# Performance work log

Hardware: AMD Instinct MI355X
Metric: run time of the kernel (lower is better)

## Reference

```python
import jax, jax.numpy as jnp
import numpy as np

B, N, C, H = 8, 4096, 512, 8
HD = C // H  # head_dim = 64
SCALE = HD ** -0.5


def setup_inputs() -> dict:
    key = jax.random.key(0)
    k1, k2, k3, k4 = jax.random.split(key, 4)
    x1 = jax.random.normal(k1, (B, N, C), dtype=jnp.float32)
    x2 = jax.random.normal(k2, (B, N, C), dtype=jnp.float32)
    # nn.Linear(dim, 2*dim, bias=False) weights; stored as [in, out] for x @ W
    lim = 1.0 / np.sqrt(C)
    W_kv1 = jax.random.uniform(k3, (C, 2 * C), dtype=jnp.float32, minval=-lim, maxval=lim)
    W_kv2 = jax.random.uniform(k4, (C, 2 * C), dtype=jnp.float32, minval=-lim, maxval=lim)
    return {"x1": x1, "x2": x2, "W_kv1": W_kv1, "W_kv2": W_kv2}


def _heads(t):
    # [B, N, C] -> [B, H, N, HD]
    return t.reshape(B, N, H, HD).transpose(0, 2, 1, 3)


def _kv(x, W):
    kv = (x @ W).reshape(B, N, 2, H, HD)  # [B, N, 2, H, HD]
    kv = kv.transpose(2, 0, 3, 1, 4)      # [2, B, H, N, HD]
    return kv[0], kv[1]


def _ctx(k, v):
    # K^T V: [B, H, HD, HD], scaled then softmax over axis -2 (the k-feature axis)
    ctx = jnp.einsum("bhnd,bhne->bhde", k, v) * SCALE
    return jax.nn.softmax(ctx, axis=-2)


def reference(x1, x2, W_kv1, W_kv2):
    q1 = _heads(x1)
    q2 = _heads(x2)
    k1, v1 = _kv(x1, W_kv1)
    k2, v2 = _kv(x2, W_kv2)
    ctx1 = _ctx(k1, v1)
    ctx2 = _ctx(k2, v2)
    # cross: q1 attends via ctx2, q2 via ctx1
    o1 = jnp.einsum("bhnd,bhde->bhne", q1, ctx2).transpose(0, 2, 1, 3).reshape(B, N, C)
    o2 = jnp.einsum("bhnd,bhde->bhne", q2, ctx1).transpose(0, 2, 1, 3).reshape(B, N, C)
    return o1, o2
```

## Files before the change

kernel.cpp:

```cpp
#include <hip/hip_runtime.h>
#include <stdint.h>
#include <stddef.h>

#define NB 8
#define NSEQ 4096
#define NC 512
#define NH 8
#define SWZ(c) ((((c) >> 2) ^ (c)) & 7)

typedef __attribute__((ext_vector_type(4))) float f4;
typedef __attribute__((ext_vector_type(8))) short bf8;
typedef __attribute__((ext_vector_type(4))) short bf4;
typedef __attribute__((ext_vector_type(2))) unsigned int u32x2;
typedef __attribute__((ext_vector_type(4))) unsigned int u32x4;

__device__ __forceinline__ short f2bf(float f) {
  union { float f; unsigned int u; } v; v.f = f;
  unsigned int u = v.u + 0x7FFFu + ((v.u >> 16) & 1u);
  return (short)(u >> 16);
}
__device__ __forceinline__ float bf2f(short h) {
  union { unsigned int u; float f; } v;
  v.u = ((unsigned int)(unsigned short)h) << 16;
  return v.f;
}
__device__ __forceinline__ unsigned int cvtpk(float a, float b) {
  unsigned int r;
  asm("v_cvt_pk_bf16_f32 %0, %1, %2" : "=v"(r) : "v"(a), "v"(b));
  return r;
}

__global__ __launch_bounds__(256) void k_wt(const float* __restrict__ W0,
                                            const float* __restrict__ W1,
                                            short* __restrict__ Wth,
                                            short* __restrict__ Wtl) {
  __shared__ float t[64 * 65];
  int bid = blockIdx.x;
  int ot = bid & 15;
  int ct = (bid >> 4) & 7;
  int s = bid >> 7;
  const float* W = s ? W1 : W0;
  const float* src = W + (size_t)(ct * 64) * 1024 + ot * 64;
  int tid = threadIdx.x;
  int rr = tid >> 4, c4 = (tid & 15) * 4;
#pragma unroll
  for (int p = 0; p < 4; ++p) {
    int c = p * 16 + rr;
    f4 v = *(const f4*)&src[(size_t)c * 1024 + c4];
#pragma unroll
    for (int i = 0; i < 4; ++i) t[(c4 + i) * 65 + c] = v[i];
  }
  __syncthreads();
  size_t obase = (size_t)s * 524288 + (size_t)(ot * 64) * 512 + ct * 64;
#pragma unroll
  for (int p = 0; p < 4; ++p) {
    int o = p * 16 + rr;
    bf4 vh, vl;
#pragma unroll
    for (int i = 0; i < 4; ++i) {
      float v = t[o * 65 + c4 + i];
      short h = f2bf(v);
      vh[i] = h; vl[i] = f2bf(v - bf2f(h));
    }
    *(bf4*)&Wth[obase + (size_t)o * 512 + c4] = vh;
    *(bf4*)&Wtl[obase + (size_t)o * 512 + c4] = vl;
  }
}

__global__ __launch_bounds__(256) void k_xbt(const float* __restrict__ x0,
                                             const float* __restrict__ x1,
                                             short* __restrict__ XbT) {
  __shared__ short t[64 * 64];
  int bx = blockIdx.x;
  int ct = bx & 7;
  int nt = (bx >> 3) & 63;
  int b  = (bx >> 9) & 7;
  int s  = bx >> 12;
  const float* x = s ? x1 : x0;
  const float* xb = x + ((size_t)b * NSEQ + (size_t)nt * 64) * NC + ct * 64;
  int tid = threadIdx.x;
  int c4 = (tid & 15) * 4;
  int nb = (tid >> 4) * 4;
  int g = nb >> 3;
  int nlo = nb & 7;
  f4 v[4];
#pragma unroll
  for (int i = 0; i < 4; ++i)
    v[i] = *(const f4*)&xb[(size_t)(nb + i) * NC + c4];
#pragma unroll
  for (int ci = 0; ci < 4; ++ci) {
    int c = c4 + ci;
    int soff = c * 64 + ((g ^ SWZ(c)) << 3) + nlo;
    u32x2 wa;
    wa[0] = cvtpk(v[0][ci], v[1][ci]);
    wa[1] = cvtpk(v[2][ci], v[3][ci]);
    *(u32x2*)&t[soff] = wa;
  }
  __syncthreads();
  int gg = tid & 7;
  int cr = tid >> 3;
  short* Xp = XbT + ((size_t)(s * 8 + b) * NC + (size_t)ct * 64) * NSEQ + (size_t)nt * 64;
#pragma unroll
  for (int p = 0; p < 2; ++p) {
    int c = cr + p * 32;
    bf8 vv = *(const bf8*)&t[c * 64 + ((gg ^ SWZ(c)) << 3)];
    *(bf8*)&Xp[(size_t)c * NSEQ + gg * 8] = vv;
  }
}

__global__ __launch_bounds__(256) void k_gram(const short* __restrict__ XbT,
                                              float* __restrict__ G32) {
  __shared__ short Ab[2][64 * 64];
  __shared__ short Bb[2][64 * 64];
  int bid = blockIdx.x;
  int xcd = bid & 7;
  int j = bid >> 3;
  int sb = xcd + ((j >= 36) ? 8 : 0);
  int p = (j >= 36) ? (j - 36) : j;
  int ti = 0;
  while (p >= 8 - ti) { p -= 8 - ti; ++ti; }
  int tj = ti + p;
  int diag = (ti == tj);
  const short* Ar = XbT + ((size_t)sb * NC + ti * 64) * NSEQ;
  const short* Br = XbT + ((size_t)sb * NC + tj * 64) * NSEQ;
  int tid = threadIdx.x;
  int lane = tid & 63;
  int w = tid >> 6;
  int lrow = lane >> 3;
  int lgr = lane & 7;
  int wr = w & 1, wc = w >> 1;
  int mrow = lane & 15;
  int kreg = lane >> 4;
  f4 z = {0.f, 0.f, 0.f, 0.f};
  f4 acc[2][2];
#pragma unroll
  for (int i = 0; i < 2; ++i)
#pragma unroll
    for (int jj = 0; jj < 2; ++jj) acc[i][jj] = z;

  auto stage = [&](int buf, int k0) {
#pragma unroll
    for (int q = 0; q < 2; ++q) {
      int r0 = q * 32 + w * 8;
      int arow = r0 + lrow;
      int gsw = (lgr ^ lrow) << 3;
      __builtin_amdgcn_global_load_lds(
          (const unsigned int*)(Ar + (size_t)arow * NSEQ + k0 + gsw),
          (unsigned int*)&Ab[buf][r0 * 64], 16, 0, 0);
      if (!diag)
        __builtin_amdgcn_global_load_lds(
            (const unsigned int*)(Br + (size_t)arow * NSEQ + k0 + gsw),
            (unsigned int*)&Bb[buf][r0 * 64], 16, 0, 0);
    }
  };
  auto comp = [&](int buf) {
    const short* Abuf = Ab[buf];
    const short* Bbuf = diag ? Ab[buf] : Bb[buf];
#pragma unroll
    for (int kk = 0; kk < 2; ++kk) {
      bf8 a[2], b[2];
      int gr = kk * 4 + kreg;
#pragma unroll
      for (int i = 0; i < 2; ++i) {
        int ra = wr * 32 + i * 16 + mrow;
        a[i] = *(const bf8*)&Abuf[ra * 64 + ((gr ^ (ra & 7)) << 3)];
        int rb2 = wc * 32 + i * 16 + mrow;
        b[i] = *(const bf8*)&Bbuf[rb2 * 64 + ((gr ^ (rb2 & 7)) << 3)];
      }
#pragma unroll
      for (int i = 0; i < 2; ++i)
#pragma unroll
        for (int jj = 0; jj < 2; ++jj)
          acc[i][jj] = __builtin_amdgcn_mfma_f32_16x16x32_bf16(a[i], b[jj], acc[i][jj], 0, 0, 0);
    }
  };

  stage(0, 0);
  __syncthreads();
  int cur = 0;
  for (int it = 0; it < 63; ++it) {
    stage(cur ^ 1, (it + 1) * 64);
    comp(cur);
    __syncthreads();
    cur ^= 1;
  }
  comp(cur);

  float* Gp = G32 + (size_t)sb * NC * NC;
  int rb = ti * 64 + wr * 32 + (lane >> 4) * 4;
  int cb = tj * 64 + wc * 32 + (lane & 15);
#pragma unroll
  for (int i = 0; i < 2; ++i)
#pragma unroll
    for (int jj = 0; jj < 2; ++jj)
#pragma unroll
      for (int r = 0; r < 4; ++r)
        Gp[(size_t)(rb + i * 16 + r) * NC + cb + jj * 16] = acc[i][jj][r];
}

__global__ __launch_bounds__(256) void k_sym(const float* __restrict__ G32,
                                             short* __restrict__ Gh,
                                             short* __restrict__ Gl) {
  __shared__ float t[64 * 65];
  int bid = blockIdx.x;
  int tile = bid & 63;
  int sb = bid >> 6;
  int ti = tile >> 3, tj = tile & 7;
  int tr = ti > tj;
  const float* src = G32 + (size_t)sb * 262144
                   + (tr ? ((size_t)(tj * 64) * 512 + ti * 64)
                         : ((size_t)(ti * 64) * 512 + tj * 64));
  int tid = threadIdx.x;
  int rr = tid >> 4;
  int c4 = (tid & 15) * 4;
#pragma unroll
  for (int p = 0; p < 4; ++p) {
    int r = p * 16 + rr;
    f4 v = *(const f4*)&src[(size_t)r * 512 + c4];
    if (tr) {
#pragma unroll
      for (int i = 0; i < 4; ++i) t[(c4 + i) * 65 + r] = v[i];
    } else {
#pragma unroll
      for (int i = 0; i < 4; ++i) t[r * 65 + c4 + i] = v[i];
    }
  }
  __syncthreads();
  size_t obase = (size_t)sb * 262144 + (size_t)(ti * 64) * 512 + tj * 64;
#pragma unroll
  for (int p = 0; p < 4; ++p) {
    int r = p * 16 + rr;
    bf4 vh, vl;
#pragma unroll
    for (int i = 0; i < 4; ++i) {
      float v = t[r * 65 + c4 + i] * 0.125f;
      short h = f2bf(v);
      vh[i] = h; vl[i] = f2bf(v - bf2f(h));
    }
    *(bf4*)&Gh[obase + (size_t)r * 512 + c4] = vh;
    *(bf4*)&Gl[obase + (size_t)r * 512 + c4] = vl;
  }
}

__global__ __launch_bounds__(256) void k_t(const short* __restrict__ Wth,
                                           const short* __restrict__ Wtl,
                                           const short* __restrict__ Gh,
                                           const short* __restrict__ Gl,
                                           float* __restrict__ Ttf) {
  __shared__ short Ah[128 * 40];
  __shared__ short Al[128 * 40];
  __shared__ short Bh[128 * 40];
  __shared__ short Bl[128 * 40];
  int tid = threadIdx.x;
  int et = blockIdx.x & 3;
  int ct = blockIdx.x >> 2;
  int sb = blockIdx.y;
  int s = sb >> 3;
  const short* Avh = Wth + ((size_t)s * 1024 + 512 + (size_t)et * 128) * NC;
  const short* Avl = Wtl + ((size_t)s * 1024 + 512 + (size_t)et * 128) * NC;
  const short* Gph = Gh + (size_t)sb * 262144 + (size_t)(ct * 128) * 512;
  const short* Gpl = Gl + (size_t)sb * 262144 + (size_t)(ct * 128) * 512;
  int cc = tid >> 1;
  int kh = (tid & 1) * 16;
  int lane = tid & 63;
  int w = tid >> 6;
  int wm = (w & 1) * 64;
  int wn = (w >> 1) * 64;
  int mrow = lane & 15;
  int kcol = (lane >> 4) * 8;
  f4 z = {0.f, 0.f, 0.f, 0.f};
  f4 acc[4][4];
#pragma unroll
  for (int i = 0; i < 4; ++i)
#pragma unroll
    for (int j = 0; j < 4; ++j) acc[i][j] = z;

  for (int it = 0; it < 16; ++it) {
    int k0 = it * 32;
    __syncthreads();
    *(bf8*)&Ah[cc * 40 + kh]     = *(const bf8*)&Avh[(size_t)cc * NC + k0 + kh];
    *(bf8*)&Ah[cc * 40 + kh + 8] = *(const bf8*)&Avh[(size_t)cc * NC + k0 + kh + 8];
    *(bf8*)&Al[cc * 40 + kh]     = *(const bf8*)&Avl[(size_t)cc * NC + k0 + kh];
    *(bf8*)&Al[cc * 40 + kh + 8] = *(const bf8*)&Avl[(size_t)cc * NC + k0 + kh + 8];
    *(bf8*)&Bh[cc * 40 + kh]     = *(const bf8*)&Gph[(size_t)cc * 512 + k0 + kh];
    *(bf8*)&Bh[cc * 40 + kh + 8] = *(const bf8*)&Gph[(size_t)cc * 512 + k0 + kh + 8];
    *(bf8*)&Bl[cc * 40 + kh]     = *(const bf8*)&Gpl[(size_t)cc * 512 + k0 + kh];
    *(bf8*)&Bl[cc * 40 + kh + 8] = *(const bf8*)&Gpl[(size_t)cc * 512 + k0 + kh + 8];
    __syncthreads();
    bf8 ah[4], al[4], bh[4], bl[4];
#pragma unroll
    for (int i = 0; i < 4; ++i) {
      ah[i] = *(const bf8*)&Ah[(wm + i * 16 + mrow) * 40 + kcol];
      al[i] = *(const bf8*)&Al[(wm + i * 16 + mrow) * 40 + kcol];
      bh[i] = *(const bf8*)&Bh[(wn + i * 16 + mrow) * 40 + kcol];
      bl[i] = *(const bf8*)&Bl[(wn + i * 16 + mrow) * 40 + kcol];
    }
#pragma unroll
    for (int i = 0; i < 4; ++i)
#pragma unroll
      for (int j = 0; j < 4; ++j) {
        acc[i][j] = __builtin_amdgcn_mfma_f32_16x16x32_bf16(ah[i], bh[j], acc[i][j], 0, 0, 0);
        acc[i][j] = __builtin_amdgcn_mfma_f32_16x16x32_bf16(ah[i], bl[j], acc[i][j], 0, 0, 0);
        acc[i][j] = __builtin_amdgcn_mfma_f32_16x16x32_bf16(al[i], bh[j], acc[i][j], 0, 0, 0);
      }
  }
  float* Tp = Ttf + (size_t)sb * NC * NC;
  int rb = et * 128 + wm + (lane >> 4) * 4;
  int cb = ct * 128 + wn + (lane & 15);
#pragma unroll
  for (int i = 0; i < 4; ++i)
#pragma unroll
    for (int j = 0; j < 4; ++j)
#pragma unroll
      for (int r = 0; r < 4; ++r)
        Tp[(size_t)(rb + i * 16 + r) * NC + cb + j * 16] = acc[i][j][r];
}

__global__ __launch_bounds__(256) void k_ctx(const short* __restrict__ Wth,
                                             const short* __restrict__ Wtl,
                                             const float* __restrict__ Ttf,
                                             short* __restrict__ ctxT) {
  __shared__ short Ah[64 * 72];
  __shared__ short Al[64 * 72];
  __shared__ short Bh[64 * 72];
  __shared__ short Bl[64 * 72];
  __shared__ float Sf[64 * 68];
  int tid = threadIdx.x;
  int h = blockIdx.x & 7;
  int sb = blockIdx.x >> 3;
  int s = sb >> 3;
  const short* Akh = Wth + ((size_t)s * 1024 + (size_t)h * 64) * NC;
  const short* Akl = Wtl + ((size_t)s * 1024 + (size_t)h * 64) * NC;
  const float* Bt = Ttf + ((size_t)sb * NC + (size_t)h * 64) * NC;
  int cs = tid >> 3;
  int kg = (tid & 7) * 8;
  int lane = tid & 63;
  int w = tid >> 6;
  int mrow = lane & 15;
  int kcol = (lane >> 4) * 8;
  f4 z = {0.f, 0.f, 0.f, 0.f};
  f4 acc[4];
#pragma unroll
  for (int j = 0; j < 4; ++j) acc[j] = z;

  for (int it = 0; it < 8; ++it) {
    int k0 = it * 64;
    __syncthreads();
#pragma unroll
    for (int r = 0; r < 2; ++r) {
      int d = cs + r * 32;
      *(bf8*)&Ah[d * 72 + kg] = *(const bf8*)&Akh[(size_t)d * NC + k0 + kg];
      *(bf8*)&Al[d * 72 + kg] = *(const bf8*)&Akl[(size_t)d * NC + k0 + kg];
      f4 g0 = *(const f4*)&Bt[(size_t)d * NC + k0 + kg];
      f4 g1 = *(const f4*)&Bt[(size_t)d * NC + k0 + kg + 4];
      bf8 vh, vl;
#pragma unroll
      for (int i = 0; i < 4; ++i) {
        short hh = f2bf(g0[i]);
        vh[i] = hh; vl[i] = f2bf(g0[i] - bf2f(hh));
        hh = f2bf(g1[i]);
        vh[i + 4] = hh; vl[i + 4] = f2bf(g1[i] - bf2f(hh));
      }
      *(bf8*)&Bh[d * 72 + kg] = vh;
      *(bf8*)&Bl[d * 72 + kg] = vl;
    }
    __syncthreads();
#pragma unroll
    for (int kk = 0; kk < 2; ++kk) {
      bf8 ah = *(const bf8*)&Ah[(w * 16 + mrow) * 72 + kk * 32 + kcol];
      bf8 al = *(const bf8*)&Al[(w * 16 + mrow) * 72 + kk * 32 + kcol];
#pragma unroll
      for (int j = 0; j < 4; ++j) {
        bf8 bh = *(const bf8*)&Bh[(j * 16 + mrow) * 72 + kk * 32 + kcol];
        bf8 bl = *(const bf8*)&Bl[(j * 16 + mrow) * 72 + kk * 32 + kcol];
        acc[j] = __builtin_amdgcn_mfma_f32_16x16x32_bf16(ah, bh, acc[j], 0, 0, 0);
        acc[j] = __builtin_amdgcn_mfma_f32_16x16x32_bf16(ah, bl, acc[j], 0, 0, 0);
        acc[j] = __builtin_amdgcn_mfma_f32_16x16x32_bf16(al, bh, acc[j], 0, 0, 0);
      }
    }
  }
  __syncthreads();
#pragma unroll
  for (int j = 0; j < 4; ++j)
#pragma unroll
    for (int r = 0; r < 4; ++r)
      Sf[(w * 16 + (lane >> 4) * 4 + r) * 68 + j * 16 + (lane & 15)] = acc[j][r];
  __syncthreads();
  if (tid < 64) {
    int e = tid;
    float mx = -1e30f;
    for (int d = 0; d < 64; ++d) mx = fmaxf(mx, Sf[d * 68 + e]);
    float sum = 0.f;
    for (int d = 0; d < 64; ++d) {
      float ev = __expf(Sf[d * 68 + e] - mx);
      sum += ev;
      Sf[d * 68 + e] = ev;
    }
    float rs = 1.f / sum;
    short* cp = ctxT + (((size_t)sb * NH + h) * 64 + e) * 64;
    for (int d0 = 0; d0 < 64; d0 += 4) {
      bf4 ov;
      ov[0] = f2bf(Sf[(d0 + 0) * 68 + e] * rs);
      ov[1] = f2bf(Sf[(d0 + 1) * 68 + e] * rs);
      ov[2] = f2bf(Sf[(d0 + 2) * 68 + e] * rs);
      ov[3] = f2bf(Sf[(d0 + 3) * 68 + e] * rs);
      *(bf4*)&cp[d0] = ov;
    }
  }
}

__global__ __launch_bounds__(256) void k_o(const float* __restrict__ x0,
                                           const float* __restrict__ x1,
                                           const short* __restrict__ ctxT,
                                           float* __restrict__ out) {
  __shared__ short Ab[128 * 72];
  __shared__ short Bb[64 * 72];
  int tid = threadIdx.x;
  int bx = blockIdx.x;
  int nt = bx & 31;
  int h = (bx >> 5) & 7;
  int b = (bx >> 8) & 7;
  int so = bx >> 11;
  const float* x = so ? x1 : x0;
  const short* cp = ctxT + (((size_t)(1 - so) * NB + b) * NH + h) * 64 * 64;
  {
    int e = tid >> 2;
    int dg = (tid & 3) * 16;
    *(bf8*)&Bb[e * 72 + dg] = *(const bf8*)&cp[e * 64 + dg];
    *(bf8*)&Bb[e * 72 + dg + 8] = *(const bf8*)&cp[e * 64 + dg + 8];
  }
  const float* xp = x + ((size_t)b * NSEQ + (size_t)nt * 128) * NC + h * 64;
  {
    int n = tid >> 1;
    int dh = (tid & 1) * 32;
    const float* row = xp + (size_t)n * NC + dh;
#pragma unroll
    for (int q = 0; q < 4; ++q) {
      f4 v0 = *(const f4*)&row[q * 8];
      f4 v1 = *(const f4*)&row[q * 8 + 4];
      u32x4 pw;
      pw[0] = cvtpk(v0[0], v0[1]);
      pw[1] = cvtpk(v0[2], v0[3]);
      pw[2] = cvtpk(v1[0], v1[1]);
      pw[3] = cvtpk(v1[2], v1[3]);
      *(u32x4*)&Ab[n * 72 + dh + q * 8] = pw;
    }
  }
  __syncthreads();
  int lane = tid & 63;
  int w = tid >> 6;
  int mrow = lane & 15;
  int kcol = (lane >> 4) * 8;
  f4 z = {0.f, 0.f, 0.f, 0.f};
  f4 acc[2][4];
#pragma unroll
  for (int i = 0; i < 2; ++i)
#pragma unroll
    for (int j = 0; j < 4; ++j) acc[i][j] = z;
#pragma unroll
  for (int kk = 0; kk < 2; ++kk) {
    bf8 a0 = *(const bf8*)&Ab[(w * 32 + mrow) * 72 + kk * 32 + kcol];
    bf8 a1 = *(const bf8*)&Ab[(w * 32 + 16 + mrow) * 72 + kk * 32 + kcol];
#pragma unroll
    for (int j = 0; j < 4; ++j) {
      bf8 bv = *(const bf8*)&Bb[(j * 16 + mrow) * 72 + kk * 32 + kcol];
      acc[0][j] = __builtin_amdgcn_mfma_f32_16x16x32_bf16(a0, bv, acc[0][j], 0, 0, 0);
      acc[1][j] = __builtin_amdgcn_mfma_f32_16x16x32_bf16(a1, bv, acc[1][j], 0, 0, 0);
    }
  }
  float* op = out + (size_t)so * ((size_t)NB * NSEQ * NC)
            + ((size_t)b * NSEQ + (size_t)nt * 128) * NC + h * 64;
#pragma unroll
  for (int i = 0; i < 2; ++i)
#pragma unroll
    for (int j = 0; j < 4; ++j)
#pragma unroll
      for (int r = 0; r < 4; ++r)
        op[(size_t)(w * 32 + i * 16 + (lane >> 4) * 4 + r) * NC + j * 16 + (lane & 15)] = acc[i][j][r];
}

extern "C" void kernel_launch(void* const* d_in, const int* in_sizes, int n_in,
                              void* d_out, int out_size, void* d_ws, size_t ws_size,
                              hipStream_t stream) {
  const float* x1 = (const float*)d_in[0];
  const float* x2 = (const float*)d_in[1];
  const float* W1 = (const float*)d_in[2];
  const float* W2 = (const float*)d_in[3];
  float* out = (float*)d_out;
  char* ws = (char*)d_ws;
  short* XbT  = (short*)ws;
  float* Ttf  = (float*)ws;
  short* Gh   = (short*)(ws + 16777216);
  short* Gl   = (short*)(ws + 25165824);
  short* Wth  = (short*)(ws + 67108864);
  short* Wtl  = (short*)(ws + 69206016);
  float* G32  = (float*)(ws + 71303168);
  short* ctxT = (short*)(ws + 88080384);

  hipLaunchKernelGGL(k_wt,   dim3(256),    dim3(256), 0, stream, W1, W2, Wth, Wtl);
  hipLaunchKernelGGL(k_xbt,  dim3(8192),   dim3(256), 0, stream, x1, x2, XbT);
  hipLaunchKernelGGL(k_gram, dim3(576),    dim3(256), 0, stream, XbT, G32);
  hipLaunchKernelGGL(k_sym,  dim3(1024),   dim3(256), 0, stream, G32, Gh, Gl);
  hipLaunchKernelGGL(k_t,    dim3(16, 16), dim3(256), 0, stream, Wth, Wtl, Gh, Gl, Ttf);
  hipLaunchKernelGGL(k_ctx,  dim3(128),    dim3(256), 0, stream, Wth, Wtl, Ttf, ctxT);
  hipLaunchKernelGGL(k_o,    dim3(4096),   dim3(256), 0, stream, x1, x2, ctxT, out);
}
```

Measured before the change: 188.6 us.

## Deepen Gram-kernel LDS pipeline to four stages and stage output stores through LDS

The Gram kernel moves from a double buffer to a four-deep ring of LDS buffers. It uses explicit vmcnt waits and raw s_barrier so that several global-to-LDS loads stay in flight while MFMAs run. The diagonal-tile special case is removed, so diagonal blocks now load the B tile redundantly. Separately, the output kernel writes its accumulators to an LDS tile first and then emits 128-bit coalesced row stores to global memory instead of scattered scalar stores. In exchange, LDS usage per block goes up, which may lower occupancy.

```diff
diff --git a/kernel.cpp b/kernel.cpp
--- a/kernel.cpp
+++ b/kernel.cpp
@@ -110,8 +110,8 @@
 
 __global__ __launch_bounds__(256) void k_gram(const short* __restrict__ XbT,
                                               float* __restrict__ G32) {
-  __shared__ short Ab[2][64 * 64];
-  __shared__ short Bb[2][64 * 64];
+  __shared__ short Ab[4][64 * 64];
+  __shared__ short Bb[4][64 * 64];
   int bid = blockIdx.x;
   int xcd = bid & 7;
   int j = bid >> 3;
@@ -120,7 +120,6 @@
   int ti = 0;
   while (p >= 8 - ti) { p -= 8 - ti; ++ti; }
   int tj = ti + p;
-  int diag = (ti == tj);
   const short* Ar = XbT + ((size_t)sb * NC + ti * 64) * NSEQ;
   const short* Br = XbT + ((size_t)sb * NC + tj * 64) * NSEQ;
   int tid = threadIdx.x;
@@ -138,7 +137,9 @@
 #pragma unroll
     for (int jj = 0; jj < 2; ++jj) acc[i][jj] = z;
 
-  auto stage = [&](int buf, int k0) {
+  auto stage = [&](int t) {
+    int buf = t & 3;
+    int k0 = t * 64;
 #pragma unroll
     for (int q = 0; q < 2; ++q) {
       int r0 = q * 32 + w * 8;
@@ -147,15 +148,14 @@
       __builtin_amdgcn_global_load_lds(
           (const unsigned int*)(Ar + (size_t)arow * NSEQ + k0 + gsw),
           (unsigned int*)&Ab[buf][r0 * 64], 16, 0, 0);
-      if (!diag)
-        __builtin_amdgcn_global_load_lds(
-            (const unsigned int*)(Br + (size_t)arow * NSEQ + k0 + gsw),
-            (unsigned int*)&Bb[buf][r0 * 64], 16, 0, 0);
+      __builtin_amdgcn_global_load_lds(
+          (const unsigned int*)(Br + (size_t)arow * NSEQ + k0 + gsw),
+          (unsigned int*)&Bb[buf][r0 * 64], 16, 0, 0);
     }
   };
   auto comp = [&](int buf) {
     const short* Abuf = Ab[buf];
-    const short* Bbuf = diag ? Ab[buf] : Bb[buf];
+    const short* Bbuf = Bb[buf];
 #pragma unroll
     for (int kk = 0; kk < 2; ++kk) {
       bf8 a[2], b[2];
@@ -175,16 +175,20 @@
     }
   };
 
-  stage(0, 0);
-  __syncthreads();
-  int cur = 0;
-  for (int it = 0; it < 63; ++it) {
-    stage(cur ^ 1, (it + 1) * 64);
-    comp(cur);
-    __syncthreads();
-    cur ^= 1;
-  }
-  comp(cur);
+  stage(0); stage(1); stage(2); stage(3);
+  for (int t = 0; t < 64; ++t) {
+    if (t < 61)       { asm volatile("s_waitcnt vmcnt(12)" ::: "memory"); }
+    else if (t == 61) { asm volatile("s_waitcnt vmcnt(8)"  ::: "memory"); }
+    else if (t == 62) { asm volatile("s_waitcnt vmcnt(4)"  ::: "memory"); }
+    else              { asm volatile("s_waitcnt vmcnt(0)"  ::: "memory"); }
+    __builtin_amdgcn_sched_barrier(0);
+    __builtin_amdgcn_s_barrier();
+    comp(t & 3);
+    asm volatile("s_waitcnt lgkmcnt(0)" ::: "memory");
+    __builtin_amdgcn_sched_barrier(0);
+    __builtin_amdgcn_s_barrier();
+    if (t + 4 < 64) stage(t + 4);
+  }
 
   float* Gp = G32 + (size_t)sb * NC * NC;
   int rb = ti * 64 + wr * 32 + (lane >> 4) * 4;
@@ -413,8 +417,10 @@
                                            const float* __restrict__ x1,
                                            const short* __restrict__ ctxT,
                                            float* __restrict__ out) {
-  __shared__ short Ab[128 * 72];
-  __shared__ short Bb[64 * 72];
+  __shared__ float U[8704];
+  short* Ab = (short*)U;
+  short* Bb = (short*)U + 128 * 72;
+  float* OutT = U;
   int tid = threadIdx.x;
   int bx = blockIdx.x;
   int nt = bx & 31;
@@ -468,15 +474,22 @@
       acc[1][j] = __builtin_amdgcn_mfma_f32_16x16x32_bf16(a1, bv, acc[1][j], 0, 0, 0);
     }
   }
-  float* op = out + (size_t)so * ((size_t)NB * NSEQ * NC)
-            + ((size_t)b * NSEQ + (size_t)nt * 128) * NC + h * 64;
+  __syncthreads();
 #pragma unroll
   for (int i = 0; i < 2; ++i)
 #pragma unroll
     for (int j = 0; j < 4; ++j)
 #pragma unroll
       for (int r = 0; r < 4; ++r)
-        op[(size_t)(w * 32 + i * 16 + (lane >> 4) * 4 + r) * NC + j * 16 + (lane & 15)] = acc[i][j][r];
+        OutT[(w * 32 + i * 16 + (lane >> 4) * 4 + r) * 68 + j * 16 + (lane & 15)] = acc[i][j][r];
+  __syncthreads();
+  int r2 = tid >> 1;
+  int ch = (tid & 1) * 32;
+  float* op2 = out + (size_t)so * ((size_t)NB * NSEQ * NC)
+             + ((size_t)b * NSEQ + (size_t)nt * 128 + r2) * NC + h * 64 + ch;
+#pragma unroll
+  for (int q = 0; q < 8; ++q)
+    *(f4*)&op2[q * 4] = *(const f4*)&OutT[r2 * 68 + ch + q * 4];
 }
 
 extern "C" void kernel_launch(void* const* d_in, const int* in_sizes, int n_in,
```

Measured after the change: 221.4 us. 17.4% more time.
